# Kernel tuning notes

Hardware: AMD Instinct MI355X
Metric: run time of the kernel (lower is better)

## Reference

```python
import jax, jax.numpy as jnp
import numpy as np
import math

D_MODEL = 1024
N_HEADS = 16
GEOM_DIM = 7
B, S = 4, 1024


def setup_inputs() -> dict:
    key = jax.random.key(0)
    ks = jax.random.split(key, 12)
    w = lambda k, shape: (jax.random.normal(k, shape, dtype=jnp.float32) * 0.02)
    return {
        "x": jax.random.normal(ks[0], (B, S, D_MODEL), dtype=jnp.float32),
        "geom_feat": jax.random.normal(ks[1], (B, S, S, GEOM_DIM), dtype=jnp.float32),
        "mask": jax.random.randint(ks[2], (B, S), 0, 2, dtype=jnp.int32),
        "Wq": w(ks[3], (D_MODEL, D_MODEL)), "bq": jnp.zeros((D_MODEL,), jnp.float32),
        "Wk": w(ks[4], (D_MODEL, D_MODEL)), "bk": jnp.zeros((D_MODEL,), jnp.float32),
        "Wv": w(ks[5], (D_MODEL, D_MODEL)), "bv": jnp.zeros((D_MODEL,), jnp.float32),
        "Wo": w(ks[6], (D_MODEL, D_MODEL)), "bo": jnp.zeros((D_MODEL,), jnp.float32),
        "Wg": w(ks[7], (GEOM_DIM, N_HEADS)), "bg": jnp.zeros((N_HEADS,), jnp.float32),
    }


def reference(x, geom_feat, mask, Wq, bq, Wk, bk, Wv, bv, Wo, bo, Wg, bg):
    b, s, d = x.shape
    h = Wg.shape[1]
    dk = d // h
    scale = math.sqrt(dk)
    # QKV projections -> [b, h, s, dk]
    Q = (x @ Wq + bq).reshape(b, s, h, dk).transpose(0, 2, 1, 3)
    K = (x @ Wk + bk).reshape(b, s, h, dk).transpose(0, 2, 1, 3)
    V = (x @ Wv + bv).reshape(b, s, h, dk).transpose(0, 2, 1, 3)
    # attention scores [b, h, s, s]
    scores = jnp.einsum("bhqd,bhkd->bhqk", Q, K) / scale
    # geometric structure bias: [b,s,s,geom_dim] -> [b,s,s,h] -> [b,h,s,s]
    struct_bias = (geom_feat @ Wg + bg).transpose(0, 3, 1, 2)
    scores = scores + struct_bias
    # key-padding mask [b, s] -> [b, 1, 1, s]
    scores = jnp.where(mask[:, None, None, :] == 0, -10000.0, scores)
    attn = jax.nn.softmax(scores, axis=-1)  # dropout disabled (eval / p=0)
    ctx = jnp.einsum("bhqk,bhkd->bhqd", attn, V)
    ctx = ctx.transpose(0, 2, 1, 3).reshape(b, s, d)
    return ctx @ Wo + bo
```

## Files before the change

kernel.cpp:

```cpp
#include <hip/hip_runtime.h>
#include <hip/hip_bf16.h>
#include <math.h>

#define BB 4
#define SS 1024
#define DD 1024
#define NH 16
#define DK 64
#define GD 7

typedef _Float16 half8 __attribute__((ext_vector_type(8)));
typedef _Float16 half4v __attribute__((ext_vector_type(4)));
typedef float floatx4 __attribute__((ext_vector_type(4)));

__device__ inline half8 cvt8(const float4 a, const float4 b) {
  half8 h;
  h[0] = (_Float16)a.x; h[1] = (_Float16)a.y; h[2] = (_Float16)a.z; h[3] = (_Float16)a.w;
  h[4] = (_Float16)b.x; h[5] = (_Float16)b.y; h[6] = (_Float16)b.z; h[7] = (_Float16)b.w;
  return h;
}

__global__ __launch_bounds__(256) void prep(const float* __restrict__ x,
                                            _Float16* __restrict__ xh,
                                            const float* __restrict__ Wq,
                                            const float* __restrict__ Wk,
                                            const float* __restrict__ Wv,
                                            const float* __restrict__ Wo,
                                            _Float16* __restrict__ Wt) {
  __shared__ _Float16 Tl[64 * 72];
  const int t = threadIdx.x;
  if (blockIdx.x < 2048) {
    const int i = blockIdx.x * 256 + t;
    const float4 a = ((const float4*)x)[i * 2];
    const float4 b = ((const float4*)x)[i * 2 + 1];
    ((half8*)xh)[i] = cvt8(a, b);
    return;
  }
  const int pf = blockIdx.x - 2048;
  const int z = pf >> 8, rem = pf & 255;
  const int n0 = (rem >> 4) * 64, k0 = (rem & 15) * 64;
  const float* src = (z == 0) ? Wq : (z == 1) ? Wk : (z == 2) ? Wv : Wo;
#pragma unroll
  for (int i = 0; i < 4; ++i) {
    const int u = i * 256 + t;
    const int r = u >> 4, c4 = (u & 15) * 4;
    const float4 v = *(const float4*)(src + (size_t)(k0 + r) * DD + n0 + c4);
    Tl[(c4 + 0) * 72 + r] = (_Float16)v.x;
    Tl[(c4 + 1) * 72 + r] = (_Float16)v.y;
    Tl[(c4 + 2) * 72 + r] = (_Float16)v.z;
    Tl[(c4 + 3) * 72 + r] = (_Float16)v.w;
  }
  __syncthreads();
  _Float16* dst = Wt + (size_t)z * DD * DD;
#pragma unroll
  for (int i = 0; i < 2; ++i) {
    const int u = i * 256 + t;
    const int nr = u >> 3, ks = u & 7;
    const half8 hv = *(const half8*)&Tl[nr * 72 + ks * 8];
    *(half8*)(dst + (size_t)(n0 + nr) * DD + k0 + ks * 8) = hv;
  }
}

template <bool PRE>
__global__ __launch_bounds__(256) void fused0(const _Float16* __restrict__ A,
                                              const _Float16* __restrict__ Bt,
                                              const float* __restrict__ bq,
                                              const float* __restrict__ bk,
                                              const float* __restrict__ bv,
                                              _Float16* __restrict__ Oq,
                                              _Float16* __restrict__ Ok,
                                              _Float16* __restrict__ Ov,
                                              const float* __restrict__ geom,
                                              const int* __restrict__ mask,
                                              const float* __restrict__ Wg,
                                              const float* __restrict__ bg,
                                              unsigned char* __restrict__ bias8) {
  const int t = threadIdx.x;
  int role, idx;
  if (PRE) {
    const int g = blockIdx.x, grp = g / 11, rem = g % 11;
    if (rem < 3) { role = 0; idx = grp * 3 + rem; }
    else         { role = 1; idx = grp * 8 + rem - 3; }
  } else {
    role = 0; idx = blockIdx.x;
  }

  if (role == 0) {
    __shared__ _Float16 Als[128 * 72];
    __shared__ _Float16 Bls[128 * 72];
    const int w = t >> 6, lane = t & 63, quad = lane >> 4, col = lane & 15;
    const int m0 = (idx & 31) * 128, n0 = (idx >> 5) * 128;
    const int mw = (w >> 1) * 64, nw = (w & 1) * 64;
    const floatx4 zero4 = {0.f, 0.f, 0.f, 0.f};
    floatx4 acc[4][4];
#pragma unroll
    for (int i = 0; i < 4; ++i)
#pragma unroll
      for (int j = 0; j < 4; ++j) acc[i][j] = zero4;

    for (int k0 = 0; k0 < DD; k0 += 64) {
#pragma unroll
      for (int i = 0; i < 4; ++i) {
        const int u = i * 256 + t;
        const int row = u >> 3, seg = u & 7;
        const half8 hv = *(const half8*)(A + (size_t)(m0 + row) * DD + k0 + seg * 8);
        *(half8*)&Als[row * 72 + seg * 8] = hv;
      }
#pragma unroll
      for (int i = 0; i < 4; ++i) {
        const int u = i * 256 + t;
        const int row = u >> 3, seg = u & 7;
        const half8 hv = *(const half8*)(Bt + (size_t)(n0 + row) * DD + k0 + seg * 8);
        *(half8*)&Bls[row * 72 + seg * 8] = hv;
      }
      __syncthreads();
#pragma unroll
      for (int kk = 0; kk < 2; ++kk) {
        half8 af[4], bf[4];
        const int u = (quad + kk * 4) * 8;
#pragma unroll
        for (int i = 0; i < 4; ++i)
          af[i] = *(const half8*)&Als[(mw + i * 16 + col) * 72 + u];
#pragma unroll
        for (int j = 0; j < 4; ++j)
          bf[j] = *(const half8*)&Bls[(nw + j * 16 + col) * 72 + u];
#pragma unroll
        for (int i = 0; i < 4; ++i)
#pragma unroll
          for (int j = 0; j < 4; ++j)
            acc[i][j] =
                __builtin_amdgcn_mfma_f32_16x16x32_f16(af[i], bf[j], acc[i][j], 0, 0, 0);
      }
      __syncthreads();
    }

#pragma unroll
    for (int j = 0; j < 4; ++j) {
      const int n = n0 + nw + j * 16 + col;
      const int which = n >> 10, hd = n & 1023;
      const int h = hd >> 6, d = hd & 63;
      const float* bp = (which == 0) ? bq : (which == 1) ? bk : bv;
      const float bias = bp[hd];
      _Float16* ob = (which == 0) ? Oq : (which == 1) ? Ok : Ov;
#pragma unroll
      for (int i = 0; i < 4; ++i) {
#pragma unroll
        for (int reg = 0; reg < 4; ++reg) {
          const int m = m0 + mw + i * 16 + quad * 4 + reg;
          const int b = m >> 10, s = m & 1023;
          ob[(((size_t)b * NH + h) * SS + s) * DK + d] = (_Float16)(acc[i][j][reg] + bias);
        }
      }
    }
    return;
  }

  if constexpr (PRE) {
    __shared__ float wgL[GD * NH + NH];
    const int r = idx;
    const int b = r >> 9;
    const int q = (r & 511) * 2 + (t >> 7);
    const int k8 = (t & 127) * 8;
    if (t < GD * NH) wgL[t] = Wg[t];
    if (t < NH) wgL[GD * NH + t] = bg[t];

    const float* gp = geom + ((size_t)b * SS + q) * SS * GD + (size_t)k8 * GD;
    float4 gv[14];
#pragma unroll
    for (int i = 0; i < 14; ++i) gv[i] = *(const float4*)(gp + i * 4);
    const float* gf = (const float*)gv;

    const int4 m4a = *(const int4*)(mask + b * SS + k8);
    const int4 m4b = *(const int4*)(mask + b * SS + k8 + 4);
    const int mk[8] = {m4a.x, m4a.y, m4a.z, m4a.w, m4b.x, m4b.y, m4b.z, m4b.w};

    __syncthreads();

    unsigned char* dst = bias8 + ((size_t)b * NH * SS + q) * SS + k8;
#pragma unroll
    for (int h = 0; h < NH; ++h) {
      float wg[GD];
#pragma unroll
      for (int g = 0; g < GD; ++g) wg[g] = wgL[g * NH + h];
      const float bgh = wgL[GD * NH + h];
      float bi[8];
#pragma unroll
      for (int k2 = 0; k2 < 8; ++k2) {
        float s = bgh;
#pragma unroll
        for (int g = 0; g < GD; ++g) s = fmaf(gf[k2 * GD + g], wg[g], s);
        bi[k2] = mk[k2] ? s : -100.f;
      }
      int w0 = 0, w1 = 0;
      w0 = __builtin_amdgcn_cvt_pk_fp8_f32(bi[0], bi[1], w0, false);
      w0 = __builtin_amdgcn_cvt_pk_fp8_f32(bi[2], bi[3], w0, true);
      w1 = __builtin_amdgcn_cvt_pk_fp8_f32(bi[4], bi[5], w1, false);
      w1 = __builtin_amdgcn_cvt_pk_fp8_f32(bi[6], bi[7], w1, true);
      uint2 u2v;
      u2v.x = (unsigned)w0;
      u2v.y = (unsigned)w1;
      *(uint2*)(dst + (size_t)h * SS * SS) = u2v;
    }
  }
}

__global__ __launch_bounds__(256) void hgemm1(const _Float16* __restrict__ A,
                                              const _Float16* __restrict__ Bt,
                                              const float* __restrict__ b0,
                                              float* __restrict__ Of) {
  __shared__ _Float16 Als[128 * 72];
  __shared__ _Float16 Bls[128 * 72];
  const int t = threadIdx.x;
  const int w = t >> 6, lane = t & 63, quad = lane >> 4, col = lane & 15;
  const int m0 = blockIdx.x * 128, n0 = blockIdx.y * 128;
  const int mw = (w >> 1) * 64, nw = (w & 1) * 64;
  const floatx4 zero4 = {0.f, 0.f, 0.f, 0.f};
  floatx4 acc[4][4];
#pragma unroll
  for (int i = 0; i < 4; ++i)
#pragma unroll
    for (int j = 0; j < 4; ++j) acc[i][j] = zero4;

  for (int k0 = 0; k0 < DD; k0 += 64) {
#pragma unroll
    for (int i = 0; i < 4; ++i) {
      const int u = i * 256 + t;
      const int row = u >> 3, seg = u & 7;
      const half8 hv = *(const half8*)(A + (size_t)(m0 + row) * DD + k0 + seg * 8);
      *(half8*)&Als[row * 72 + seg * 8] = hv;
    }
#pragma unroll
    for (int i = 0; i < 4; ++i) {
      const int u = i * 256 + t;
      const int row = u >> 3, seg = u & 7;
      const half8 hv = *(const half8*)(Bt + (size_t)(n0 + row) * DD + k0 + seg * 8);
      *(half8*)&Bls[row * 72 + seg * 8] = hv;
    }
    __syncthreads();
#pragma unroll
    for (int kk = 0; kk < 2; ++kk) {
      half8 af[4], bf[4];
      const int u = (quad + kk * 4) * 8;
#pragma unroll
      for (int i = 0; i < 4; ++i) af[i] = *(const half8*)&Als[(mw + i * 16 + col) * 72 + u];
#pragma unroll
      for (int j = 0; j < 4; ++j) bf[j] = *(const half8*)&Bls[(nw + j * 16 + col) * 72 + u];
#pragma unroll
      for (int i = 0; i < 4; ++i)
#pragma unroll
        for (int j = 0; j < 4; ++j)
          acc[i][j] = __builtin_amdgcn_mfma_f32_16x16x32_f16(af[i], bf[j], acc[i][j], 0, 0, 0);
    }
    __syncthreads();
  }

#pragma unroll
  for (int j = 0; j < 4; ++j) {
    const int n = n0 + nw + j * 16 + col;
    const float bias = b0[n];
#pragma unroll
    for (int i = 0; i < 4; ++i) {
#pragma unroll
      for (int reg = 0; reg < 4; ++reg) {
        const int m = m0 + mw + i * 16 + quad * 4 + reg;
        Of[(size_t)m * DD + n] = acc[i][j][reg] + bias;
      }
    }
  }
}

template <bool PREBIAS>
__global__ __launch_bounds__(256) void attn(const _Float16* __restrict__ Q,
                                            const _Float16* __restrict__ K,
                                            const _Float16* __restrict__ V,
                                            const unsigned char* __restrict__ bias8,
                                            const float* __restrict__ geom,
                                            const int* __restrict__ mask,
                                            const float* __restrict__ Wg,
                                            const float* __restrict__ bg,
                                            _Float16* __restrict__ ctxbuf) {
  __shared__ _Float16 Ks[64 * 64];
  __shared__ _Float16 Vt[64 * 72];
  __shared__ unsigned char biasL[PREBIAS ? 64 * 80 : 64 * 144];
  __shared__ _Float16 pL[4 * 16 * 72];
  __shared__ unsigned char mskL[SS];

  const int t = threadIdx.x;
  const int w = t >> 6, lane = t & 63, quad = lane >> 4, col = lane & 15;
  const int h = blockIdx.x, qt = blockIdx.y, b = blockIdx.z;
  const int q0 = qt * 64;
  const size_t bh = (size_t)b * NH + h;
  const _Float16* Qb = Q + bh * SS * DK;
  const _Float16* Kb = K + bh * SS * DK;
  const _Float16* Vb = V + bh * SS * DK;
  _Float16* biasLf = (_Float16*)biasL;

  {
    const int j = t >> 2, u2 = (t & 3) * 2;
    const half8 h0 = *(const half8*)(Qb + (size_t)(q0 + j) * DK + u2 * 8);
    const half8 h1 = *(const half8*)(Qb + (size_t)(q0 + j) * DK + u2 * 8 + 8);
    *(half8*)&Ks[(j * 8 + (u2 ^ (j & 7))) * 8] = h0;
    *(half8*)&Ks[(j * 8 + ((u2 + 1) ^ (j & 7))) * 8] = h1;
  }
  if constexpr (!PREBIAS) {
    const int4 m4 = *(const int4*)(mask + b * SS + t * 4);
    mskL[t * 4 + 0] = m4.x != 0;
    mskL[t * 4 + 1] = m4.y != 0;
    mskL[t * 4 + 2] = m4.z != 0;
    mskL[t * 4 + 3] = m4.w != 0;
  }
  __syncthreads();
  half8 qfrag[2];
  {
    const int qrow = w * 16 + col;
#pragma unroll
    for (int kk = 0; kk < 2; ++kk) {
      const int u = quad + kk * 4;
      qfrag[kk] = *(const half8*)&Ks[(qrow * 8 + (u ^ (qrow & 7))) * 8];
    }
  }

  float wgv[GD];
  float bgh = 0.f;
  const float* gptr = nullptr;
  if constexpr (!PREBIAS) {
#pragma unroll
    for (int g = 0; g < GD; ++g) wgv[g] = Wg[g * NH + h];
    bgh = bg[h];
    gptr = geom + (((size_t)b * SS + (q0 + (t >> 2))) * SS + (t & 3) * 16) * GD;
  }
  const unsigned char* bb8 = nullptr;
  if constexpr (PREBIAS) bb8 = bias8 + (bh * SS + q0) * SS;

  const floatx4 zero4 = {0.f, 0.f, 0.f, 0.f};
  floatx4 ctx[4] = {zero4, zero4, zero4, zero4};
  float lsum[4] = {0.f, 0.f, 0.f, 0.f};
  _Float16* pW = &pL[w * 16 * 72];

  for (int c = 0; c < 16; ++c) {
    const int k0 = c * 64;
    __syncthreads();

    {
      const int j = t >> 2, u2 = (t & 3) * 2;
      const half8 h0 = *(const half8*)(Kb + (size_t)(k0 + j) * DK + u2 * 8);
      const half8 h1 = *(const half8*)(Kb + (size_t)(k0 + j) * DK + u2 * 8 + 8);
      *(half8*)&Ks[(j * 8 + (u2 ^ (j & 7))) * 8] = h0;
      *(half8*)&Ks[(j * 8 + ((u2 + 1) ^ (j & 7))) * 8] = h1;
    }
    {
      const int kg = (t >> 4) * 4, dg = (t & 15) * 4;
      half4v f[4];
#pragma unroll
      for (int e = 0; e < 4; ++e)
        f[e] = *(const half4v*)(Vb + (size_t)(k0 + kg + e) * DK + dg);
#pragma unroll
      for (int i = 0; i < 4; ++i) {
        half4v hv = {f[0][i], f[1][i], f[2][i], f[3][i]};
        *(half4v*)&Vt[(dg + i) * 72 + kg] = hv;
      }
    }
    if constexpr (PREBIAS) {
      const int row = t >> 2, seg = (t & 3) * 16;
      const uint4 v = *(const uint4*)(bb8 + (size_t)row * SS + k0 + seg);
      *(uint4*)&biasL[row * 80 + seg] = v;
    } else {
      const int gq = t >> 2, gk = (t & 3) * 16;
#pragma unroll
      for (int sg = 0; sg < 4; ++sg) {
        float4 gvv[7];
#pragma unroll
        for (int i7 = 0; i7 < 7; ++i7) gvv[i7] = *(const float4*)(gptr + sg * 28 + i7 * 4);
        const float* gf = (const float*)gvv;
        half4v bv;
#pragma unroll
        for (int k2 = 0; k2 < 4; ++k2) {
          float bi = bgh;
#pragma unroll
          for (int g = 0; g < GD; ++g) bi = fmaf(gf[k2 * GD + g], wgv[g], bi);
          bv[k2] = mskL[k0 + gk + sg * 4 + k2] ? (_Float16)bi : (_Float16)(-100.f);
        }
        *(half4v*)&biasLf[gq * 72 + gk + sg * 4] = bv;
      }
      gptr += 64 * GD;
    }
    __syncthreads();

    floatx4 sc[4] = {zero4, zero4, zero4, zero4};
#pragma unroll
    for (int nt = 0; nt < 4; ++nt) {
      const int key = nt * 16 + col;
#pragma unroll
      for (int kk = 0; kk < 2; ++kk) {
        const int u = quad + kk * 4;
        const half8 kf = *(const half8*)&Ks[(key * 8 + (u ^ (key & 7))) * 8];
        sc[nt] = __builtin_amdgcn_mfma_f32_16x16x32_f16(qfrag[kk], kf, sc[nt], 0, 0, 0);
      }
    }

#pragma unroll
    for (int nt = 0; nt < 4; ++nt) {
#pragma unroll
      for (int reg = 0; reg < 4; ++reg) {
        const int q = quad * 4 + reg;
        float bias;
        if constexpr (PREBIAS) {
          bias = __builtin_amdgcn_cvt_f32_fp8(
              (int)biasL[(w * 16 + q) * 80 + nt * 16 + col], 0);
        } else {
          bias = (float)biasLf[(w * 16 + q) * 72 + nt * 16 + col];
        }
        const float s = fmaf(sc[nt][reg], 0.125f, bias);
        const float p = __expf(s);
        lsum[reg] += p;
        pW[q * 72 + nt * 16 + col] = (_Float16)p;
      }
    }

#pragma unroll
    for (int kk = 0; kk < 2; ++kk) {
      const half8 pa = *(const half8*)&pW[col * 72 + quad * 8 + kk * 32];
#pragma unroll
      for (int nt = 0; nt < 4; ++nt) {
        const half8 vb = *(const half8*)&Vt[(nt * 16 + col) * 72 + quad * 8 + kk * 32];
        ctx[nt] = __builtin_amdgcn_mfma_f32_16x16x32_f16(pa, vb, ctx[nt], 0, 0, 0);
      }
    }
  }

  float inv[4];
#pragma unroll
  for (int reg = 0; reg < 4; ++reg) {
    float l = lsum[reg];
    l += __shfl_xor(l, 1, 64);
    l += __shfl_xor(l, 2, 64);
    l += __shfl_xor(l, 4, 64);
    l += __shfl_xor(l, 8, 64);
    inv[reg] = 1.f / l;
  }
#pragma unroll
  for (int nt = 0; nt < 4; ++nt) {
#pragma unroll
    for (int reg = 0; reg < 4; ++reg) {
      const int q = q0 + w * 16 + quad * 4 + reg;
      ctxbuf[((size_t)b * SS + q) * DD + h * DK + nt * 16 + col] =
          (_Float16)(ctx[nt][reg] * inv[reg]);
    }
  }
}

extern "C" void kernel_launch(void* const* d_in, const int* in_sizes, int n_in,
                              void* d_out, int out_size, void* d_ws, size_t ws_size,
                              hipStream_t stream) {
  const float* x    = (const float*)d_in[0];
  const float* geom = (const float*)d_in[1];
  const int*   mask = (const int*)d_in[2];
  const float* Wq   = (const float*)d_in[3];
  const float* bq   = (const float*)d_in[4];
  const float* Wk   = (const float*)d_in[5];
  const float* bk   = (const float*)d_in[6];
  const float* Wv   = (const float*)d_in[7];
  const float* bv   = (const float*)d_in[8];
  const float* Wo   = (const float*)d_in[9];
  const float* bo   = (const float*)d_in[10];
  const float* Wg   = (const float*)d_in[11];
  const float* bg   = (const float*)d_in[12];
  float* out = (float*)d_out;

  const size_t NEL = (size_t)BB * SS * DD;
  char* p = (char*)d_ws;
  _Float16* xh   = (_Float16*)p;            p += NEL * 2;
  _Float16* Wt   = (_Float16*)p;            p += NEL * 2;
  _Float16* Qh   = (_Float16*)p;            p += NEL * 2;
  _Float16* Kh   = (_Float16*)p;            p += NEL * 2;
  _Float16* Vh   = (_Float16*)p;            p += NEL * 2;
  _Float16* ctxh = (_Float16*)p;            p += NEL * 2;
  unsigned char* bias8 = (unsigned char*)p;
  const size_t need = (size_t)48 * 1024 * 1024 + (size_t)BB * NH * SS * SS;
  const bool prebias = ws_size >= need;

  prep<<<3072, 256, 0, stream>>>(x, xh, Wq, Wk, Wv, Wo, Wt);

  if (prebias) {
    fused0<true><<<2816, 256, 0, stream>>>(xh, Wt, bq, bk, bv, Qh, Kh, Vh,
                                           geom, mask, Wg, bg, bias8);
    attn<true><<<dim3(NH, SS / 64, BB), 256, 0, stream>>>(Qh, Kh, Vh, bias8, geom, mask,
                                                          Wg, bg, ctxh);
  } else {
    fused0<false><<<768, 256, 0, stream>>>(xh, Wt, bq, bk, bv, Qh, Kh, Vh,
                                           geom, mask, Wg, bg, nullptr);
    attn<false><<<dim3(NH, SS / 64, BB), 256, 0, stream>>>(Qh, Kh, Vh, nullptr, geom, mask,
                                                           Wg, bg, ctxh);
  }

  hgemm1<<<dim3(32, 8), 256, 0, stream>>>(ctxh, Wt + (size_t)3 * DD * DD, bo, out);
}
```

Measured before the change: 337.8 us.

## Store fp8 bias in MFMA fragment order and load directly into registers

The precomputed fp8 geometric bias is now written in a layout matching the MFMA accumulator fragment order. Each attention thread loads one 32-bit word per tile straight from global memory, instead of staging the bias through shared memory. The bias-producing blocks now handle four query rows per thread with 16-byte stores, which changes the block-role interleaving in the fused kernel. The 1/sqrt(dk) scale is folded into Q at projection time, removing a multiply per score. The cost is scattered, less coalesced per-lane 4-byte global loads in the attention loop, and extra register pressure in the producer.

After: 368.1 us. +9.0%, slower.

```diff
diff --git a/kernel.cpp b/kernel.cpp
--- a/kernel.cpp
+++ b/kernel.cpp
@@ -74,13 +74,13 @@
                                               const int* __restrict__ mask,
                                               const float* __restrict__ Wg,
                                               const float* __restrict__ bg,
-                                              unsigned char* __restrict__ bias8) {
+                                              unsigned* __restrict__ bias8) {
   const int t = threadIdx.x;
   int role, idx;
   if (PRE) {
-    const int g = blockIdx.x, grp = g / 11, rem = g % 11;
+    const int g = blockIdx.x, grp = g / 7, rem = g % 7;
     if (rem < 3) { role = 0; idx = grp * 3 + rem; }
-    else         { role = 1; idx = grp * 8 + rem - 3; }
+    else         { role = 1; idx = grp * 4 + rem - 3; }
   } else {
     role = 0; idx = blockIdx.x;
   }
@@ -141,6 +141,7 @@
       const int h = hd >> 6, d = hd & 63;
       const float* bp = (which == 0) ? bq : (which == 1) ? bk : bv;
       const float bias = bp[hd];
+      const float scale = (which == 0) ? 0.125f : 1.f;
       _Float16* ob = (which == 0) ? Oq : (which == 1) ? Ok : Ov;
 #pragma unroll
       for (int i = 0; i < 4; ++i) {
@@ -148,7 +149,8 @@
         for (int reg = 0; reg < 4; ++reg) {
           const int m = m0 + mw + i * 16 + quad * 4 + reg;
           const int b = m >> 10, s = m & 1023;
-          ob[(((size_t)b * NH + h) * SS + s) * DK + d] = (_Float16)(acc[i][j][reg] + bias);
+          ob[(((size_t)b * NH + h) * SS + s) * DK + d] =
+              (_Float16)((acc[i][j][reg] + bias) * scale);
         }
       }
     }
@@ -158,48 +160,53 @@
   if constexpr (PRE) {
     __shared__ float wgL[GD * NH + NH];
     const int r = idx;
-    const int b = r >> 9;
-    const int q = (r & 511) * 2 + (t >> 7);
-    const int k8 = (t & 127) * 8;
+    const int b = r >> 8;
+    const int rg = r & 255;
+    const int qt = rg >> 4, wv = (rg >> 2) & 3, quad = rg & 3;
+    const int k0 = t * 4;
+    const int c = k0 >> 6, nt = (k0 & 63) >> 4, colb = k0 & 15;
     if (t < GD * NH) wgL[t] = Wg[t];
     if (t < NH) wgL[GD * NH + t] = bg[t];
 
-    const float* gp = geom + ((size_t)b * SS + q) * SS * GD + (size_t)k8 * GD;
-    float4 gv[14];
-#pragma unroll
-    for (int i = 0; i < 14; ++i) gv[i] = *(const float4*)(gp + i * 4);
+    float4 gv[28];
+#pragma unroll
+    for (int qr = 0; qr < 4; ++qr) {
+      const float* gp = geom + (((size_t)b * SS + rg * 4 + qr) * SS + k0) * GD;
+#pragma unroll
+      for (int i = 0; i < 7; ++i) gv[qr * 7 + i] = *(const float4*)(gp + i * 4);
+    }
     const float* gf = (const float*)gv;
-
-    const int4 m4a = *(const int4*)(mask + b * SS + k8);
-    const int4 m4b = *(const int4*)(mask + b * SS + k8 + 4);
-    const int mk[8] = {m4a.x, m4a.y, m4a.z, m4a.w, m4b.x, m4b.y, m4b.z, m4b.w};
-
+    const int4 m4 = *(const int4*)(mask + b * SS + k0);
+    const int mk[4] = {m4.x, m4.y, m4.z, m4.w};
     __syncthreads();
 
-    unsigned char* dst = bias8 + ((size_t)b * NH * SS + q) * SS + k8;
+    const size_t base0 = (size_t)(b * NH) * 262144 + (size_t)qt * 16384 +
+                         (size_t)c * 1024 + (size_t)wv * 256 + (size_t)nt * 64 +
+                         quad * 16 + colb;
 #pragma unroll
     for (int h = 0; h < NH; ++h) {
       float wg[GD];
 #pragma unroll
       for (int g = 0; g < GD; ++g) wg[g] = wgL[g * NH + h];
       const float bgh = wgL[GD * NH + h];
-      float bi[8];
-#pragma unroll
-      for (int k2 = 0; k2 < 8; ++k2) {
-        float s = bgh;
-#pragma unroll
-        for (int g = 0; g < GD; ++g) s = fmaf(gf[k2 * GD + g], wg[g], s);
-        bi[k2] = mk[k2] ? s : -100.f;
-      }
-      int w0 = 0, w1 = 0;
-      w0 = __builtin_amdgcn_cvt_pk_fp8_f32(bi[0], bi[1], w0, false);
-      w0 = __builtin_amdgcn_cvt_pk_fp8_f32(bi[2], bi[3], w0, true);
-      w1 = __builtin_amdgcn_cvt_pk_fp8_f32(bi[4], bi[5], w1, false);
-      w1 = __builtin_amdgcn_cvt_pk_fp8_f32(bi[6], bi[7], w1, true);
-      uint2 u2v;
-      u2v.x = (unsigned)w0;
-      u2v.y = (unsigned)w1;
-      *(uint2*)(dst + (size_t)h * SS * SS) = u2v;
+      unsigned u[4];
+#pragma unroll
+      for (int e = 0; e < 4; ++e) {
+        float bi[4];
+#pragma unroll
+        for (int qr = 0; qr < 4; ++qr) {
+          float s = bgh;
+#pragma unroll
+          for (int g = 0; g < GD; ++g) s = fmaf(gf[qr * 28 + e * 7 + g], wg[g], s);
+          bi[qr] = mk[e] ? s : -100.f;
+        }
+        int wd = 0;
+        wd = __builtin_amdgcn_cvt_pk_fp8_f32(bi[0], bi[1], wd, false);
+        wd = __builtin_amdgcn_cvt_pk_fp8_f32(bi[2], bi[3], wd, true);
+        u[e] = (unsigned)wd;
+      }
+      uint4 uv = {u[0], u[1], u[2], u[3]};
+      *(uint4*)(bias8 + base0 + (size_t)h * 262144) = uv;
     }
   }
 }
@@ -273,7 +280,7 @@
 __global__ __launch_bounds__(256) void attn(const _Float16* __restrict__ Q,
                                             const _Float16* __restrict__ K,
                                             const _Float16* __restrict__ V,
-                                            const unsigned char* __restrict__ bias8,
+                                            const unsigned* __restrict__ bias8,
                                             const float* __restrict__ geom,
                                             const int* __restrict__ mask,
                                             const float* __restrict__ Wg,
@@ -281,9 +288,9 @@
                                             _Float16* __restrict__ ctxbuf) {
   __shared__ _Float16 Ks[64 * 64];
   __shared__ _Float16 Vt[64 * 72];
-  __shared__ unsigned char biasL[PREBIAS ? 64 * 80 : 64 * 144];
   __shared__ _Float16 pL[4 * 16 * 72];
-  __shared__ unsigned char mskL[SS];
+  __shared__ _Float16 biasLf[PREBIAS ? 8 : 64 * 72];
+  __shared__ unsigned char mskL[PREBIAS ? 8 : SS];
 
   const int t = threadIdx.x;
   const int w = t >> 6, lane = t & 63, quad = lane >> 4, col = lane & 15;
@@ -293,7 +300,6 @@
   const _Float16* Qb = Q + bh * SS * DK;
   const _Float16* Kb = K + bh * SS * DK;
   const _Float16* Vb = V + bh * SS * DK;
-  _Float16* biasLf = (_Float16*)biasL;
 
   {
     const int j = t >> 2, u2 = (t & 3) * 2;
@@ -329,8 +335,7 @@
     bgh = bg[h];
     gptr = geom + (((size_t)b * SS + (q0 + (t >> 2))) * SS + (t & 3) * 16) * GD;
   }
-  const unsigned char* bb8 = nullptr;
-  if constexpr (PREBIAS) bb8 = bias8 + (bh * SS + q0) * SS;
+  const size_t bbase = PREBIAS ? ((bh * 16 + (size_t)qt) * 16384 + (size_t)w * 256 + lane) : 0;
 
   const floatx4 zero4 = {0.f, 0.f, 0.f, 0.f};
   floatx4 ctx[4] = {zero4, zero4, zero4, zero4};
@@ -339,6 +344,14 @@
 
   for (int c = 0; c < 16; ++c) {
     const int k0 = c * 64;
+
+    unsigned bw[4];
+    if constexpr (PREBIAS) {
+#pragma unroll
+      for (int nt = 0; nt < 4; ++nt)
+        bw[nt] = bias8[bbase + (size_t)c * 1024 + nt * 64];
+    }
+
     __syncthreads();
 
     {
@@ -360,11 +373,7 @@
         *(half4v*)&Vt[(dg + i) * 72 + kg] = hv;
       }
     }
-    if constexpr (PREBIAS) {
-      const int row = t >> 2, seg = (t & 3) * 16;
-      const uint4 v = *(const uint4*)(bb8 + (size_t)row * SS + k0 + seg);
-      *(uint4*)&biasL[row * 80 + seg] = v;
-    } else {
+    if constexpr (!PREBIAS) {
       const int gq = t >> 2, gk = (t & 3) * 16;
 #pragma unroll
       for (int sg = 0; sg < 4; ++sg) {
@@ -400,18 +409,23 @@
 
 #pragma unroll
     for (int nt = 0; nt < 4; ++nt) {
+      floatx4 b4;
+      if constexpr (PREBIAS) {
+        b4[0] = __builtin_amdgcn_cvt_f32_fp8((int)bw[nt], 0);
+        b4[1] = __builtin_amdgcn_cvt_f32_fp8((int)bw[nt], 1);
+        b4[2] = __builtin_amdgcn_cvt_f32_fp8((int)bw[nt], 2);
+        b4[3] = __builtin_amdgcn_cvt_f32_fp8((int)bw[nt], 3);
+      }
 #pragma unroll
       for (int reg = 0; reg < 4; ++reg) {
         const int q = quad * 4 + reg;
         float bias;
         if constexpr (PREBIAS) {
-          bias = __builtin_amdgcn_cvt_f32_fp8(
-              (int)biasL[(w * 16 + q) * 80 + nt * 16 + col], 0);
+          bias = b4[reg];
         } else {
           bias = (float)biasLf[(w * 16 + q) * 72 + nt * 16 + col];
         }
-        const float s = fmaf(sc[nt][reg], 0.125f, bias);
-        const float p = __expf(s);
+        const float p = __expf(sc[nt][reg] + bias);
         lsum[reg] += p;
         pW[q * 72 + nt * 16 + col] = (_Float16)p;
       }
@@ -475,14 +489,14 @@
   _Float16* Kh   = (_Float16*)p;            p += NEL * 2;
   _Float16* Vh   = (_Float16*)p;            p += NEL * 2;
   _Float16* ctxh = (_Float16*)p;            p += NEL * 2;
-  unsigned char* bias8 = (unsigned char*)p;
+  unsigned* bias8 = (unsigned*)p;
   const size_t need = (size_t)48 * 1024 * 1024 + (size_t)BB * NH * SS * SS;
   const bool prebias = ws_size >= need;
 
   prep<<<3072, 256, 0, stream>>>(x, xh, Wq, Wk, Wv, Wo, Wt);
 
   if (prebias) {
-    fused0<true><<<2816, 256, 0, stream>>>(xh, Wt, bq, bk, bv, Qh, Kh, Vh,
+    fused0<true><<<1792, 256, 0, stream>>>(xh, Wt, bq, bk, bv, Qh, Kh, Vh,
                                            geom, mask, Wg, bg, bias8);
     attn<true><<<dim3(NH, SS / 64, BB), 256, 0, stream>>>(Qh, Kh, Vh, bias8, geom, mask,
                                                           Wg, bg, ctxh);
```
